# Kernel optimization log

Hardware: AMD Instinct MI355X
Metric: run time of the kernel (lower is better)

Reference implementation:

```python
import jax, jax.numpy as jnp
import numpy as np

T, B, E, H, DFF, K = 1024, 4, 512, 8, 2048, 31
D = E // H  # head_dim


def double_swish(x):
    # DoubleSwish: x * sigmoid(x - 1)
    return x * jax.nn.sigmoid(x - 1.0)


def ffn(x, w1, b1, w2, b2):
    # ScaledLinear -> ActivationBalancer(identity in eval) -> DoubleSwish -> ScaledLinear
    return double_swish(x @ w1.T + b1) @ w2.T + b2


def rel_shift(x):
    # x: (B, H, T, 2T-1) -> (B, H, T, T); out[b,h,i,j] = x[b,h,i, (T-1) - i + j]
    t = x.shape[2]
    idx = (t - 1) - jnp.arange(t)[:, None] + jnp.arange(t)[None, :]  # (T, T)
    return jnp.take_along_axis(x, idx[None, None], axis=-1)


def self_attn(x, pos_emb, wqkv, bqkv, wo, bo, wpos, u, v):
    # x: (T, B, E); Transformer-XL style rel-pos multi-head attention
    t, b, e = x.shape
    qkv = x @ wqkv.T + bqkv                       # (T, B, 3E)
    q, k, val = jnp.split(qkv, 3, axis=-1)
    q = q * (D ** -0.5)
    to_heads = lambda z: z.reshape(t, b, H, D).transpose(1, 2, 0, 3)  # (B,H,T,D)
    q, k, val = to_heads(q), to_heads(k), to_heads(val)
    # positional projection: (1, 2T-1, E) -> (1, H, D, 2T-1)
    p = (pos_emb @ wpos.T).reshape(1, 2 * t - 1, H, D).transpose(0, 2, 3, 1)
    ac = jnp.einsum('bhld,bhsd->bhls', q + u[None, :, None, :], k)
    bd = jnp.einsum('bhld,bhdm->bhlm', q + v[None, :, None, :], p)
    scores = ac + rel_shift(bd)                   # (B, H, T, T)
    attn = jax.nn.softmax(scores, axis=-1)
    out = jnp.einsum('bhls,bhsd->bhld', attn, val)
    out = out.transpose(2, 0, 1, 3).reshape(t, b, e)  # (T, B, E)
    return out @ wo.T + bo


def conv_module(x, pw1_w, pw1_b, dw_w, dw_b, pw2_w, pw2_b):
    # x: (T, B, C) -> (B, C, T)
    x = x.transpose(1, 2, 0)
    x = jnp.einsum('oc,bct->bot', pw1_w, x) + pw1_b[None, :, None]  # (B, 2C, T)
    a, g = jnp.split(x, 2, axis=1)
    x = a * jax.nn.sigmoid(g)                     # GLU over channel dim
    pad = (K - 1) // 2
    x = jax.lax.conv_general_dilated(
        x, dw_w, window_strides=(1,), padding=[(pad, pad)],
        dimension_numbers=('NCH', 'OIH', 'NCH'), feature_group_count=E)
    x = double_swish(x + dw_b[None, :, None])
    x = jnp.einsum('oc,bct->bot', pw2_w, x) + pw2_b[None, :, None]
    return x.transpose(2, 0, 1)                   # (T, B, C)


def basic_norm(x, log_eps):
    # BasicNorm: x * (mean(x^2, -1) + exp(eps))^{-0.5}
    return x * jax.lax.rsqrt(jnp.mean(x * x, axis=-1, keepdims=True) + jnp.exp(log_eps))


def setup_inputs() -> dict:
    key = jax.random.key(0)
    ks = jax.random.split(key, 24)
    std = jnp.float32(0.02)
    f = lambda k, s: jax.random.normal(k, s, jnp.float32)
    return dict(
        src=f(ks[0], (T, B, E)),
        pos_emb=f(ks[1], (1, 2 * T - 1, E)),
        in_proj_w=f(ks[2], (3 * E, E)) * std,
        in_proj_b=f(ks[3], (3 * E,)) * std,
        out_proj_w=f(ks[4], (E, E)) * std,
        out_proj_b=f(ks[5], (E,)) * std,
        linear_pos_w=f(ks[6], (E, E)) * std,
        pos_bias_u=f(ks[7], (H, D)) * jnp.float32(0.01),
        pos_bias_v=f(ks[8], (H, D)) * jnp.float32(0.01),
        ffm_w1=f(ks[9], (DFF, E)) * std, ffm_b1=f(ks[10], (DFF,)) * std,
        ffm_w2=f(ks[11], (E, DFF)) * std, ffm_b2=f(ks[12], (E,)) * std,
        ff_w1=f(ks[13], (DFF, E)) * std, ff_b1=f(ks[14], (DFF,)) * std,
        ff_w2=f(ks[15], (E, DFF)) * std, ff_b2=f(ks[16], (E,)) * std,
        conv_pw1_w=f(ks[17], (2 * E, E)) * std, conv_pw1_b=f(ks[18], (2 * E,)) * std,
        conv_dw_w=f(ks[19], (E, 1, K)) * std, conv_dw_b=f(ks[20], (E,)) * std,
        conv_pw2_w=f(ks[21], (E, E)) * std, conv_pw2_b=f(ks[22], (E,)) * std,
        norm_eps=jnp.array(np.log(0.25), jnp.float32),
    )


def reference(src, pos_emb, in_proj_w, in_proj_b, out_proj_w, out_proj_b,
              linear_pos_w, pos_bias_u, pos_bias_v,
              ffm_w1, ffm_b1, ffm_w2, ffm_b2,
              ff_w1, ff_b1, ff_w2, ff_b2,
              conv_pw1_w, conv_pw1_b, conv_dw_w, conv_dw_b, conv_pw2_w, conv_pw2_b,
              norm_eps):
    # macaron FFN
    x = src + ffn(src, ffm_w1, ffm_b1, ffm_w2, ffm_b2)
    # rel-pos self-attention
    x = x + self_attn(x, pos_emb, in_proj_w, in_proj_b, out_proj_w, out_proj_b,
                      linear_pos_w, pos_bias_u, pos_bias_v)
    # convolution module
    x = x + conv_module(x, conv_pw1_w, conv_pw1_b, conv_dw_w, conv_dw_b, conv_pw2_w, conv_pw2_b)
    # second FFN
    x = x + ffn(x, ff_w1, ff_b1, ff_w2, ff_b2)
    # balancer is identity in eval; final BasicNorm
    return basic_norm(x, norm_eps)
```

## Files before the change

kernel.cpp:

```cpp
#include <hip/hip_runtime.h>
#include <string.h>


#define T_ 1024
#define B_ 4
#define E_ 512
#define H_ 8
#define DFF_ 2048
#define KW_ 31

typedef unsigned short u16;
typedef unsigned int u32;
typedef __bf16 bf16x8 __attribute__((ext_vector_type(8)));
typedef float floatx4 __attribute__((ext_vector_type(4)));

__device__ __forceinline__ float b2f(u16 u) {
    return __uint_as_float(((u32)u) << 16);
}
__device__ __forceinline__ u16 f2b(float f) {
    u32 i = __float_as_uint(f);
    u32 r = (i + 0x7fffu + ((i >> 16) & 1u)) >> 16;
    return (u16)r;
}

__device__ __forceinline__ void glds16(const u16 *g, u16 *l) {
    __builtin_amdgcn_global_load_lds((const __attribute__((address_space(1))) void *)g,
                                     (__attribute__((address_space(3))) void *)l, 16, 0, 0);
}

__global__ __launch_bounds__(256) void fill_k(float *out, long long n, float val) {
    long long g = (long long)blockIdx.x * 256 + threadIdx.x;
    if (g < n) out[g] = val;
}

__global__ __launch_bounds__(256) void detect_k(const u16 *src16, int *flag) {
    __shared__ int sh[256];
    int tid = threadIdx.x;
    int cnt = 0;
    for (int i = tid; i < 4096; i += 256) {
        u16 x = src16[2 * i];
        int e = (x >> 7) & 0xFF;
        cnt += (e == 0 || (e >= 0x70 && e <= 0x8F)) ? 1 : 0;
    }
    sh[tid] = cnt;
    __syncthreads();
    for (int s = 128; s; s >>= 1) {
        if (tid < s) sh[tid] += sh[tid + s];
        __syncthreads();
    }
    if (tid == 0) *flag = (sh[0] < 2048) ? 1 : 0;
}

struct CVT {
    const void *in[24];
    long long pre[25];
};

__global__ __launch_bounds__(256) void convert_k(CVT c, u16 *dst, const int *flag,
                                                 long long total) {
    long long g = (long long)blockIdx.x * 256 + threadIdx.x;
    if (g >= total) return;
    int s = 0;
#pragma unroll
    for (int i = 1; i < 25; i++) s += (g >= c.pre[i]) ? 1 : 0;
    long long l = g - c.pre[s];
    int f = *flag;
    u16 v = f ? f2b(((const float *)c.in[s])[l]) : ((const u16 *)c.in[s])[l];
    dst[g] = v;
}

struct GP {
    const u16 *A, *B;
    u16 *C;
    const u16 *bias;
    const void *resin;
    float *xr;
    u16 *xb;
    const u16 *ub, *vb;
    u16 *qu, *qv, *kh, *vt;
    int M, N, K, lda, ldb, ldc, mode, qcols, resin_f32;
    float qscale;
};

__global__ __launch_bounds__(512) void gemm_nt(GP p) {
    __shared__ __align__(16) u16 As[3 * 4096];
    __shared__ __align__(16) u16 Bs[3 * 4096];
    const int tid = threadIdx.x;
    const int wv = tid >> 6, ln = tid & 63;
    const int l16 = ln & 15, quad = ln >> 4;
    const int wm = (wv >> 2) << 5;
    const int wn = (wv & 3) << 4;
    const int gx = gridDim.x;
    const int nb = gx * gridDim.y;
    const int lid = blockIdx.y * gx + blockIdx.x;
    const int nid = (lid & 7) * (nb >> 3) + (lid >> 3);
    const int m0 = (nid / gx) << 6, n0 = (nid % gx) << 6;
    floatx4 zero = {0.f, 0.f, 0.f, 0.f};
    floatx4 acc[2];
    acc[0] = zero;
    acc[1] = zero;

    const int NT = p.K >> 6;

    const int srow = tid >> 3;
    const int sg = ((tid & 7) ^ (srow & 7)) << 3;
    int ra = m0 + srow;
    if (ra > p.M - 1) ra = p.M - 1;
    const u16 *Agp = p.A + (long long)ra * p.lda + sg;
    const u16 *Bgp = p.B + (long long)(n0 + srow) * p.ldb + sg;

    auto stage = [&](int bidx, int t) {
        const int k0 = t << 6;
        const int o = bidx << 12;
        glds16(Agp + k0, As + o + tid * 8);
        glds16(Bgp + k0, Bs + o + tid * 8);
    };

    stage(0, 0);
    stage(1, 1);
    stage(2, 2);
    asm volatile("s_waitcnt vmcnt(4)" ::: "memory");
    __builtin_amdgcn_s_barrier();

    int cb = 0;
    for (int t = 0; t < NT; t++) {
        const int o = cb << 12;
#pragma unroll
        for (int kk = 0; kk < 2; kk++) {
            const int swz = ((((kk << 2) | quad) ^ (l16 & 7)) << 3);
            bf16x8 bfv = __builtin_bit_cast(bf16x8,
                *(const uint4 *)&Bs[o + ((wn + l16) << 6) + swz]);
#pragma unroll
            for (int mt = 0; mt < 2; mt++) {
                bf16x8 af = __builtin_bit_cast(bf16x8,
                    *(const uint4 *)&As[o + ((wm + (mt << 4) + l16) << 6) + swz]);
                acc[mt] = __builtin_amdgcn_mfma_f32_16x16x32_bf16(af, bfv, acc[mt], 0, 0, 0);
            }
        }
        if (t + 1 < NT) {
            __builtin_amdgcn_sched_barrier(0);
            __builtin_amdgcn_s_barrier();
            if (t + 3 < NT) {
                stage(cb, t + 3);
                asm volatile("s_waitcnt vmcnt(4)" ::: "memory");
            } else if (t + 2 < NT) {
                asm volatile("s_waitcnt vmcnt(2)" ::: "memory");
            } else {
                asm volatile("s_waitcnt vmcnt(0)" ::: "memory");
            }
            __builtin_amdgcn_s_barrier();
            __builtin_amdgcn_sched_barrier(0);
        }
        cb = (cb == 2) ? 0 : cb + 1;
    }

#pragma unroll
    for (int mt = 0; mt < 2; mt++) {
#pragma unroll
        for (int r = 0; r < 4; r++) {
            int gr = m0 + wm + (mt << 4) + (quad << 2) + r;
            int gc = n0 + wn + l16;
            bool oob = gr >= p.M;
            if (oob && p.mode != 3) continue;
            float y = 0.f;
            if (!oob) {
                y = acc[mt][r];
                if (p.bias) y += b2f(p.bias[gc]);
                if (gc < p.qcols) y *= p.qscale;
            }
            if (p.mode == 3) {
                p.C[((gc >> 6) << 17) + (gr << 6) + (gc & 63)] = f2b(y);
            } else if (p.mode == 0) {
                p.C[(long long)gr * p.ldc + gc] = f2b(y);
            } else if (p.mode == 1) {
                float s = 1.f / (1.f + __expf(1.f - y));
                p.C[(long long)gr * p.ldc + gc] = f2b(y * s);
            } else {
                long long idx = (long long)gr * p.ldc + gc;
                float rv = p.resin_f32 ? ((const float *)p.resin)[idx]
                                       : b2f(((const u16 *)p.resin)[idx]);
                float o = rv + y;
                p.xr[idx] = o;
                if (p.xb) p.xb[idx] = f2b(o);
            }
        }
    }
}

__global__ __launch_bounds__(512) void gemm_nt128(GP p) {
    __shared__ __align__(16) u16 As[3 * 4096];
    __shared__ __align__(16) u16 Bs[3 * 4096];
    const int tid = threadIdx.x;
    const int wv = tid >> 6, ln = tid & 63;
    const int l16 = ln & 15, quad = ln >> 4;
    const int wm = (wv >> 2) << 6;
    const int wn = (wv & 3) << 5;
    const int gx = gridDim.x;
    const int nb = gx * gridDim.y;
    const int lid = blockIdx.y * gx + blockIdx.x;
    const int nid = (lid & 7) * (nb >> 3) + (lid >> 3);
    const int m0 = (nid / gx) << 7, n0 = (nid % gx) << 7;
    const int srow = tid >> 2;
    const int sg = ((tid & 3) ^ ((tid >> 3) & 3)) << 3;
    const u16 *Agp = p.A + (long long)(m0 + srow) * p.lda + sg;
    const u16 *Bgp = p.B + (long long)(n0 + srow) * p.ldb + sg;
    floatx4 zero = {0.f, 0.f, 0.f, 0.f};
    floatx4 acc[4][2];
#pragma unroll
    for (int i = 0; i < 4; i++)
#pragma unroll
        for (int j = 0; j < 2; j++) acc[i][j] = zero;

    const int rswz = ((quad ^ ((l16 >> 1) & 3)) << 3);
    const int NT = p.K >> 5;

    auto stage = [&](int bidx, int t) {
        const int k0 = t << 5;
        const int o = bidx << 12;
        glds16(Agp + k0, As + o + tid * 8);
        glds16(Bgp + k0, Bs + o + tid * 8);
    };

    stage(0, 0);
    stage(1, 1);
    stage(2, 2);
    asm volatile("s_waitcnt vmcnt(4)" ::: "memory");
    __builtin_amdgcn_s_barrier();

    int cb = 0;
    for (int t = 0; t < NT; t++) {
        const int o = cb << 12;
        bf16x8 av[4], bv[2];
#pragma unroll
        for (int mt = 0; mt < 4; mt++)
            av[mt] = __builtin_bit_cast(bf16x8,
                *(const uint4 *)&As[o + ((wm + (mt << 4) + l16) << 5) + rswz]);
#pragma unroll
        for (int nt = 0; nt < 2; nt++)
            bv[nt] = __builtin_bit_cast(bf16x8,
                *(const uint4 *)&Bs[o + ((wn + (nt << 4) + l16) << 5) + rswz]);
#pragma unroll
        for (int mt = 0; mt < 4; mt++)
#pragma unroll
            for (int nt = 0; nt < 2; nt++)
                acc[mt][nt] = __builtin_amdgcn_mfma_f32_16x16x32_bf16(av[mt], bv[nt],
                                                                      acc[mt][nt], 0, 0, 0);
        if (t + 1 < NT) {
            __builtin_amdgcn_sched_barrier(0);
            __builtin_amdgcn_s_barrier();
            if (t + 3 < NT) {
                stage(cb, t + 3);
                asm volatile("s_waitcnt vmcnt(4)" ::: "memory");
            } else if (t + 2 < NT) {
                asm volatile("s_waitcnt vmcnt(2)" ::: "memory");
            } else {
                asm volatile("s_waitcnt vmcnt(0)" ::: "memory");
            }
            __builtin_amdgcn_s_barrier();
            __builtin_amdgcn_sched_barrier(0);
        }
        cb = (cb == 2) ? 0 : cb + 1;
    }

#pragma unroll
    for (int mt = 0; mt < 4; mt++)
#pragma unroll
        for (int nt = 0; nt < 2; nt++)
#pragma unroll
            for (int r = 0; r < 4; r++) {
                int gr = m0 + wm + (mt << 4) + (quad << 2) + r;
                int gc = n0 + wn + (nt << 4) + l16;
                float y = acc[mt][nt][r];
                if (p.bias) y += b2f(p.bias[gc]);
                if (gc < p.qcols) y *= p.qscale;
                if (p.mode == 0) {
                    p.C[(long long)gr * p.ldc + gc] = f2b(y);
                } else if (p.mode == 1) {
                    float s = 1.f / (1.f + __expf(1.f - y));
                    p.C[(long long)gr * p.ldc + gc] = f2b(y * s);
                } else if (p.mode == 4) {
                    int t = gr >> 2, b = gr & 3;
                    if (gc < E_) {
                        int z = b * 8 + (gc >> 6);
                        long long oq = ((long long)z << 16) + (t << 6) + (gc & 63);
                        p.qu[oq] = f2b(y + b2f(p.ub[gc]));
                        p.qv[oq] = f2b(y + b2f(p.vb[gc]));
                    } else if (gc < 2 * E_) {
                        int c = gc - E_;
                        int z = b * 8 + (c >> 6);
                        p.kh[((long long)z << 16) + (t << 6) + (c & 63)] = f2b(y);
                    } else {
                        int c = gc - 2 * E_;
                        int z = b * 8 + (c >> 6);
                        p.vt[(long long)((z << 6) + (c & 63)) * T_ + t] = f2b(y);
                    }
                } else {
                    long long idx = (long long)gr * p.ldc + gc;
                    float rv = p.resin_f32 ? ((const float *)p.resin)[idx]
                                           : b2f(((const u16 *)p.resin)[idx]);
                    float o = rv + y;
                    p.xr[idx] = o;
                    if (p.xb) p.xb[idx] = f2b(o);
                }
            }
}

__global__ __launch_bounds__(512) void gemm_glu(const u16 *A, const u16 *W, const u16 *bias,
                                                u16 *ch) {
    __shared__ __align__(16) u16 As[3 * 4096];
    __shared__ __align__(16) u16 Ba[3 * 4096];
    __shared__ __align__(16) u16 Bg[3 * 4096];
    const int tid = threadIdx.x;
    const int wv = tid >> 6, ln = tid & 63;
    const int l16 = ln & 15, quad = ln >> 4;
    const int wm = (wv >> 2) << 5;
    const int wn = (wv & 3) << 4;
    const int gx = gridDim.x;
    const int nb = gx * gridDim.y;
    const int lid = blockIdx.y * gx + blockIdx.x;
    const int nid = (lid & 7) * (nb >> 3) + (lid >> 3);
    const int m0 = (nid / gx) << 6, n0 = (nid % gx) << 6;
    floatx4 zero = {0.f, 0.f, 0.f, 0.f};
    floatx4 aa[2], ag[2];
    aa[0] = zero; aa[1] = zero; ag[0] = zero; ag[1] = zero;

    const int NT = 8;
    const int srow = tid >> 3;
    const int sg = ((tid & 7) ^ (srow & 7)) << 3;
    const u16 *Agp = A + ((long long)(m0 + srow) << 9) + sg;
    const u16 *Bap = W + ((long long)(n0 + srow) << 9) + sg;
    const u16 *Bgp = W + ((long long)(E_ + n0 + srow) << 9) + sg;

    auto stage = [&](int bidx, int t) {
        const int k0 = t << 6;
        const int o = bidx << 12;
        glds16(Agp + k0, As + o + tid * 8);
        glds16(Bap + k0, Ba + o + tid * 8);
        glds16(Bgp + k0, Bg + o + tid * 8);
    };

    stage(0, 0);
    stage(1, 1);
    stage(2, 2);
    asm volatile("s_waitcnt vmcnt(6)" ::: "memory");
    __builtin_amdgcn_s_barrier();

    int cb = 0;
    for (int t = 0; t < NT; t++) {
        const int o = cb << 12;
#pragma unroll
        for (int kk = 0; kk < 2; kk++) {
            const int swz = ((((kk << 2) | quad) ^ (l16 & 7)) << 3);
            bf16x8 ba = __builtin_bit_cast(bf16x8,
                *(const uint4 *)&Ba[o + ((wn + l16) << 6) + swz]);
            bf16x8 bg = __builtin_bit_cast(bf16x8,
                *(const uint4 *)&Bg[o + ((wn + l16) << 6) + swz]);
#pragma unroll
            for (int mt = 0; mt < 2; mt++) {
                bf16x8 af = __builtin_bit_cast(bf16x8,
                    *(const uint4 *)&As[o + ((wm + (mt << 4) + l16) << 6) + swz]);
                aa[mt] = __builtin_amdgcn_mfma_f32_16x16x32_bf16(af, ba, aa[mt], 0, 0, 0);
                ag[mt] = __builtin_amdgcn_mfma_f32_16x16x32_bf16(af, bg, ag[mt], 0, 0, 0);
            }
        }
        if (t + 1 < NT) {
            __builtin_amdgcn_sched_barrier(0);
            __builtin_amdgcn_s_barrier();
            if (t + 3 < NT) {
                stage(cb, t + 3);
                asm volatile("s_waitcnt vmcnt(6)" ::: "memory");
            } else if (t + 2 < NT) {
                asm volatile("s_waitcnt vmcnt(3)" ::: "memory");
            } else {
                asm volatile("s_waitcnt vmcnt(0)" ::: "memory");
            }
            __builtin_amdgcn_s_barrier();
            __builtin_amdgcn_sched_barrier(0);
        }
        cb = (cb == 2) ? 0 : cb + 1;
    }

#pragma unroll
    for (int mt = 0; mt < 2; mt++) {
#pragma unroll
        for (int r = 0; r < 4; r++) {
            int gr = m0 + wm + (mt << 4) + (quad << 2) + r;
            int gc = n0 + wn + l16;
            float a = aa[mt][r] + b2f(bias[gc]);
            float g = ag[mt][r] + b2f(bias[E_ + gc]);
            ch[((long long)gr << 9) + gc] = f2b(a * (1.f / (1.f + __expf(-g))));
        }
    }
}

struct FK {
    const u16 *QU, *QV, *KH, *PPH, *VT;
    u16 *attno;
};

__global__ __launch_bounds__(256) void flash_k(FK p) {
    __shared__ __align__(16) u16 lds[25088];
    u16 *Kh = lds;
    u16 *Ph = lds + 4096;
    u16 *Pb = lds + 20480;

    const int tid = threadIdx.x;
    const int wv = tid >> 6, ln = tid & 63;
    const int l16 = ln & 15, quad = ln >> 4;
    const int lid = blockIdx.y * 16 + blockIdx.x;
    const int nid = (lid & 7) * 64 + (lid >> 3);
    const int zg = nid >> 4;
    const int i0 = (nid & 15) << 6;
    const u16 *kh0 = p.KH + (long long)zg * 65536;
    const u16 *ph0 = p.PPH + (long long)(zg & 7) * 131072;
    const u16 *vt0 = p.VT + (long long)zg * 65536;

    auto stage_kp = [&](int jt) {
        const int j0 = jt << 6;
        const int m_start = 960 - i0 + j0;
#pragma unroll
        for (int ps = 0; ps < 2; ps++) {
            int g = ps * 256 + tid;
            int row = g >> 3;
            int src = ((g & 7) ^ (row & 7)) << 3;
            glds16(kh0 + ((j0 + row) << 6) + src, Kh + g * 8);
        }
#pragma unroll
        for (int ps = 0; ps < 4; ps++) {
            int g = ps * 256 + tid;
            int row = g >> 3;
            int src = ((g & 7) ^ (row & 7)) << 3;
            glds16(ph0 + ((m_start + row) << 6) + src, Ph + g * 8);
        }
    };
    auto stage_v = [&](int buf, int jt) {
        const int j0 = jt << 6;
        u16 *Vt = lds + 12288 + (buf << 12);
#pragma unroll
        for (int ps = 0; ps < 2; ps++) {
            int g = ps * 256 + tid;
            int row = g >> 3;
            int src = ((g & 7) ^ (row & 7)) << 3;
            glds16(vt0 + (row << 10) + j0 + src, Vt + g * 8);
        }
    };

    const long long qoff = (long long)zg * 65536 + (long long)(i0 + (wv << 4) + l16) * 64 + (quad << 3);
    bf16x8 aqu[2], aqv[2];
#pragma unroll
    for (int kk = 0; kk < 2; kk++) {
        aqu[kk] = __builtin_bit_cast(bf16x8, *(const uint4 *)(p.QU + qoff + (kk << 5)));
        aqv[kk] = __builtin_bit_cast(bf16x8, *(const uint4 *)(p.QV + qoff + (kk << 5)));
    }

    stage_kp(0);
    stage_v(0, 0);
    asm volatile("s_waitcnt vmcnt(0)" ::: "memory");
    __builtin_amdgcn_s_barrier();

    float lacc[4];
    floatx4 accO[4];
    floatx4 zero = {0.f, 0.f, 0.f, 0.f};
#pragma unroll
    for (int e = 0; e < 4; e++) lacc[e] = 0.f;
#pragma unroll
    for (int i = 0; i < 4; i++) accO[i] = zero;

    const int r16q = quad << 2;

    for (int jt = 0; jt < 16; jt++) {
        floatx4 aS[4], aB[5];
#pragma unroll
        for (int i = 0; i < 4; i++) aS[i] = zero;
#pragma unroll
        for (int i = 0; i < 5; i++) aB[i] = zero;
        __builtin_amdgcn_s_setprio(1);
#pragma unroll
        for (int kk = 0; kk < 2; kk++) {
            const int swz = ((((kk << 2) | quad) ^ (l16 & 7)) << 3);
#pragma unroll
            for (int nt = 0; nt < 4; nt++) {
                bf16x8 bf = __builtin_bit_cast(bf16x8,
                    *(const uint4 *)&Kh[(((nt << 4) | l16) << 6) + swz]);
                aS[nt] = __builtin_amdgcn_mfma_f32_16x16x32_bf16(aqu[kk], bf, aS[nt], 0, 0, 0);
            }
#pragma unroll
            for (int rt = 0; rt < 5; rt++) {
                bf16x8 bf = __builtin_bit_cast(bf16x8,
                    *(const uint4 *)&Ph[((((rt + 3 - wv) << 4) | l16) << 6) + swz]);
                aB[rt] = __builtin_amdgcn_mfma_f32_16x16x32_bf16(aqv[kk], bf, aB[rt], 0, 0, 0);
            }
        }
        __builtin_amdgcn_s_setprio(0);
        __builtin_amdgcn_sched_barrier(0);
        __builtin_amdgcn_s_barrier();
        if (jt + 1 < 16) {
            stage_kp(jt + 1);
            stage_v((jt + 1) & 1, jt + 1);
        }
        __builtin_amdgcn_sched_barrier(0);

#pragma unroll
        for (int e = 0; e < 4; e++) {
            const int r16 = r16q + e;
            const int t = l16 + 15 - r16;
            const int srcl = (quad << 4) | (t & 15);
            const int carry = t >> 4;
            float s5[5];
#pragma unroll
            for (int rt = 0; rt < 5; rt++) s5[rt] = __shfl(aB[rt][e], srcl, 64);
            float ps = 0.f;
#pragma unroll
            for (int nt = 0; nt < 4; nt++) {
                float bd = carry ? s5[nt + 1] : s5[nt];
                float pe = __expf(aS[nt][e] + bd);
                ps += pe;
                Pb[(((wv << 4) + r16) * 72) + (nt << 4) + l16] = f2b(pe);
            }
            lacc[e] += ps;
        }

        const u16 *Vt = lds + 12288 + ((jt & 1) << 12);
        __builtin_amdgcn_s_setprio(1);
#pragma unroll
        for (int kk = 0; kk < 2; kk++) {
            const int swz = ((((kk << 2) | quad) ^ (l16 & 7)) << 3);
            bf16x8 ap = __builtin_bit_cast(bf16x8,
                *(const uint4 *)&Pb[(((wv << 4) | l16) * 72) + (kk << 5) + (quad << 3)]);
#pragma unroll
            for (int nd = 0; nd < 4; nd++) {
                bf16x8 bv = __builtin_bit_cast(bf16x8,
                    *(const uint4 *)&Vt[(((nd << 4) | l16) << 6) + swz]);
                accO[nd] = __builtin_amdgcn_mfma_f32_16x16x32_bf16(ap, bv, accO[nd], 0, 0, 0);
            }
        }
        __builtin_amdgcn_s_setprio(0);

        if (jt + 1 < 16) {
            __builtin_amdgcn_sched_barrier(0);
            asm volatile("s_waitcnt vmcnt(0)" ::: "memory");
            __builtin_amdgcn_s_barrier();
            __builtin_amdgcn_sched_barrier(0);
        }
    }

    const int b = zg >> 3, h = zg & 7;
#pragma unroll
    for (int e = 0; e < 4; e++) {
#pragma unroll
        for (int msk = 1; msk < 16; msk <<= 1) lacc[e] += __shfl_xor(lacc[e], msk, 64);
        float inv = 1.f / lacc[e];
        int t = i0 + (wv << 4) + (quad << 2) + e;
#pragma unroll
        for (int nd = 0; nd < 4; nd++) {
            int d = (nd << 4) + l16;
            p.attno[(long long)(t * B_ + b) * E_ + h * 64 + d] = f2b(accO[nd][e] * inv);
        }
    }
}


__global__ __launch_bounds__(256) void dwconv_k(const u16 *ch, const u16 *w, const u16 *bias,
                                                u16 *cd) {
    const int cp = threadIdx.x;
    const int b = blockIdx.x >> 7;
    const int t0 = (blockIdx.x & 127) << 3;
    const int c0 = cp << 1;
    float in0[38], in1[38];
#pragma unroll
    for (int j = 0; j < 38; j++) {
        int tt = t0 - 15 + j;
        u32 v = 0;
        if (tt >= 0 && tt < T_) v = *(const u32 *)&ch[tt * 2048 + b * 512 + c0];
        in0[j] = b2f((u16)(v & 0xffff));
        in1[j] = b2f((u16)(v >> 16));
    }
    float w0[KW_], w1[KW_];
#pragma unroll
    for (int kk = 0; kk < KW_; kk++) {
        w0[kk] = b2f(w[c0 * KW_ + kk]);
        w1[kk] = b2f(w[c0 * KW_ + KW_ + kk]);
    }
    float bi0 = b2f(bias[c0]), bi1 = b2f(bias[c0 + 1]);
#pragma unroll
    for (int t = 0; t < 8; t++) {
        float a0 = bi0, a1 = bi1;
#pragma unroll
        for (int kk = 0; kk < KW_; kk++) {
            a0 += in0[t + kk] * w0[kk];
            a1 += in1[t + kk] * w1[kk];
        }
        float s0 = 1.f / (1.f + __expf(1.f - a0));
        float s1 = 1.f / (1.f + __expf(1.f - a1));
        u32 o = (u32)f2b(a0 * s0) | ((u32)f2b(a1 * s1) << 16);
        *(u32 *)&cd[(t0 + t) * 2048 + b * 512 + c0] = o;
    }
}

__global__ __launch_bounds__(256) void norm_k(const float *xr, const float *epsp, float *out) {
    int wv = threadIdx.x >> 6, ln = threadIdx.x & 63;
    long long row = blockIdx.x * 4 + wv;
    const float *x = xr + row * E_;
    float vals[8], ss = 0.f;
#pragma unroll
    for (int i = 0; i < 8; i++) {
        vals[i] = x[ln + (i << 6)];
        ss += vals[i] * vals[i];
    }
#pragma unroll
    for (int m = 32; m; m >>= 1) ss += __shfl_xor(ss, m, 64);
    float sc = rsqrtf(ss * (1.f / (float)E_) + __expf(epsp[0]));
    float *o = out + row * E_;
#pragma unroll
    for (int i = 0; i < 8; i++) o[ln + (i << 6)] = vals[i] * sc;
}


extern "C" void kernel_launch(void *const *d_in, const int *in_sizes, int n_in,
                              void *d_out, int out_size, void *d_ws, size_t ws_size,
                              hipStream_t stream) {
    const size_t MB = (size_t)1 << 20;
    static const long long EXPECT[24] = {
        2097152, 1048064, 786432, 1536, 262144, 512, 262144, 512, 512,
        1048576, 2048, 1048576, 512, 1048576, 2048, 1048576, 512,
        524288, 1024, 15872, 512, 262144, 512, 1};
    const size_t NEED = 93 * MB;

    float code = 0.f;
    if (n_in != 24) {
        code = 1000.f + (float)n_in;
    } else {
        for (int i = 0; i < 24; i++) {
            if ((long long)in_sizes[i] != EXPECT[i]) { code = 2000.f + 64.f * i; break; }
        }
    }
    if (code == 0.f && out_size != 2097152) code = 3000.f;
    if (code == 0.f && ws_size < NEED) code = 5000.f + (float)(ws_size / MB);
    if (code != 0.f) {
        long long n = (long long)out_size;
        fill_k<<<dim3((unsigned)((n + 255) / 256)), dim3(256), 0, stream>>>((float *)d_out, n, code);
        return;
    }

    char *w = (char *)d_ws;
    int *flag = (int *)(w + 0);
    u16 *cv = (u16 *)(w + 1 * MB);
    float *xr = (float *)(w + 21 * MB);
    u16 *xb = (u16 *)(w + 29 * MB);
    u16 *h1 = (u16 *)(w + 33 * MB);
    u16 *pph = (u16 *)(w + 63 * MB);
    u16 *QU = (u16 *)(w + 65 * MB);
    u16 *QV = (u16 *)(w + 69 * MB);
    u16 *KH = (u16 *)(w + 73 * MB);
    u16 *VT = (u16 *)(w + 77 * MB);
    u16 *attno = (u16 *)(w + 81 * MB);
    u16 *ch = (u16 *)(w + 85 * MB);
    u16 *cd = (u16 *)(w + 89 * MB);

    detect_k<<<dim3(1), dim3(256), 0, stream>>>((const u16 *)d_in[0], flag);
    CVT c;
    c.pre[0] = 0;
    for (int i = 0; i < 24; i++) {
        c.in[i] = d_in[i];
        c.pre[i + 1] = c.pre[i] + in_sizes[i];
    }
    long long total = c.pre[24];
    convert_k<<<dim3((unsigned)((total + 255) / 256)), dim3(256), 0, stream>>>(c, cv, flag, total);

    const u16 *src = cv + c.pre[0];
    const u16 *pos_emb = cv + c.pre[1];
    const u16 *w_qkv = cv + c.pre[2];
    const u16 *b_qkv = cv + c.pre[3];
    const u16 *w_o = cv + c.pre[4];
    const u16 *b_o = cv + c.pre[5];
    const u16 *w_pos = cv + c.pre[6];
    const u16 *u_bias = cv + c.pre[7];
    const u16 *v_bias = cv + c.pre[8];
    const u16 *ffm_w1 = cv + c.pre[9];
    const u16 *ffm_b1 = cv + c.pre[10];
    const u16 *ffm_w2 = cv + c.pre[11];
    const u16 *ffm_b2 = cv + c.pre[12];
    const u16 *ff_w1 = cv + c.pre[13];
    const u16 *ff_b1 = cv + c.pre[14];
    const u16 *ff_w2 = cv + c.pre[15];
    const u16 *ff_b2 = cv + c.pre[16];
    const u16 *pw1_w = cv + c.pre[17];
    const u16 *pw1_b = cv + c.pre[18];
    const u16 *dw_w = cv + c.pre[19];
    const u16 *dw_b = cv + c.pre[20];
    const u16 *pw2_w = cv + c.pre[21];
    const u16 *pw2_b = cv + c.pre[22];

    auto mk = [](const void *A, int lda, const void *B, int ldb, void *C, int ldc,
                 const void *bias, int M, int N, int K, int mode) {
        GP p;
        memset(&p, 0, sizeof(p));
        p.A = (const u16 *)A; p.B = (const u16 *)B; p.C = (u16 *)C; p.bias = (const u16 *)bias;
        p.M = M; p.N = N; p.K = K; p.lda = lda; p.ldb = ldb; p.ldc = ldc; p.mode = mode;
        p.qscale = 1.f;
        return p;
    };
    auto launch = [&](GP p) {
        dim3 g((p.N + 63) / 64, (p.M + 63) / 64, 1);
        gemm_nt<<<g, dim3(512), 0, stream>>>(p);
    };
    auto launch128 = [&](GP p) {
        dim3 g(p.N >> 7, p.M >> 7, 1);
        gemm_nt128<<<g, dim3(512), 0, stream>>>(p);
    };

    const int M = T_ * B_;

    { GP p = mk(src, E_, ffm_w1, E_, h1, DFF_, ffm_b1, M, DFF_, E_, 1); launch128(p); }
    { GP p = mk(h1, DFF_, ffm_w2, DFF_, nullptr, E_, ffm_b2, M, E_, DFF_, 2);
      p.resin = d_in[0]; p.resin_f32 = 1; p.xr = xr; p.xb = xb; launch(p); }

    { GP p = mk(xb, E_, w_qkv, E_, nullptr, 3 * E_, b_qkv, M, 3 * E_, E_, 4);
      p.qcols = E_; p.qscale = 0.125f;
      p.ub = u_bias; p.vb = v_bias; p.qu = QU; p.qv = QV; p.kh = KH; p.vt = VT;
      launch128(p); }
    { GP p = mk(pos_emb, E_, w_pos, E_, pph, E_, nullptr, 2 * T_ - 1, E_, E_, 3); launch(p); }

    {
        FK f;
        f.QU = QU; f.QV = QV; f.KH = KH; f.PPH = pph; f.VT = VT; f.attno = attno;
        flash_k<<<dim3(16, 32), dim3(256), 0, stream>>>(f);
    }

    { GP p = mk(attno, E_, w_o, E_, nullptr, E_, b_o, M, E_, E_, 2);
      p.resin = xr; p.resin_f32 = 1; p.xr = xr; p.xb = xb; launch(p); }

    gemm_glu<<<dim3(8, 64), dim3(512), 0, stream>>>(xb, pw1_w, pw1_b, ch);
    dwconv_k<<<dim3(512), dim3(256), 0, stream>>>(ch, dw_w, dw_b, cd);
    { GP p = mk(cd, E_, pw2_w, E_, nullptr, E_, pw2_b, M, E_, E_, 2);
      p.resin = xr; p.resin_f32 = 1; p.xr = xr; p.xb = xb; launch(p); }

    { GP p = mk(xb, E_, ff_w1, E_, h1, DFF_, ff_b1, M, DFF_, E_, 1); launch128(p); }
    { GP p = mk(h1, DFF_, ff_w2, DFF_, nullptr, E_, ff_b2, M, E_, DFF_, 2);
      p.resin = xr; p.resin_f32 = 1; p.xr = xr; p.xb = nullptr; launch(p); }

    norm_k<<<dim3(M / 4), dim3(256), 0, stream>>>(xr, (const float *)d_in[23], (float *)d_out);
}
```

Before: 373.1 us.

## Split attention KV range across two blocks and combine partials

The flash attention kernel now splits the 1024 keys into two halves handled by separate blocks, doubling the grid to 1024 blocks. Each block writes unnormalised fp32 partial outputs and row sums, and a new combine kernel adds the halves and normalises. The positional tile is now loaded straight from global memory into registers instead of through LDS, and K/V staging is issued at the top of each iteration. This raises occupancy and parallelism on a grid that was small relative to the CU count, at the cost of an extra launch and a round trip of partial results through memory. Reusing the h1 buffer for the partials relies on h1 being dead at that point.

Result: slower. 411.8 us (+10.4%).

```diff
diff --git a/kernel.cpp b/kernel.cpp
--- a/kernel.cpp
+++ b/kernel.cpp
@@ -395,54 +395,58 @@
 
 struct FK {
     const u16 *QU, *QV, *KH, *PPH, *VT;
-    u16 *attno;
+    float *Op;
+    float *lp;
 };
 
 __global__ __launch_bounds__(256) void flash_k(FK p) {
-    __shared__ __align__(16) u16 lds[25088];
-    u16 *Kh = lds;
-    u16 *Ph = lds + 4096;
-    u16 *Pb = lds + 20480;
+    __shared__ __align__(16) u16 lds[20992];
+    u16 *Pb = lds + 16384;
 
     const int tid = threadIdx.x;
     const int wv = tid >> 6, ln = tid & 63;
     const int l16 = ln & 15, quad = ln >> 4;
-    const int lid = blockIdx.y * 16 + blockIdx.x;
-    const int nid = (lid & 7) * 64 + (lid >> 3);
-    const int zg = nid >> 4;
+    const int lid = blockIdx.y * 32 + blockIdx.x;
+    const int nid = (lid & 7) * 128 + (lid >> 3);
+    const int zg = nid >> 5;
+    const int kvh = (nid >> 4) & 1;
     const int i0 = (nid & 15) << 6;
+    const int jt0 = kvh << 3;
     const u16 *kh0 = p.KH + (long long)zg * 65536;
     const u16 *ph0 = p.PPH + (long long)(zg & 7) * 131072;
     const u16 *vt0 = p.VT + (long long)zg * 65536;
 
-    auto stage_kp = [&](int jt) {
+    auto stage_k = [&](int buf, int jt) {
         const int j0 = jt << 6;
-        const int m_start = 960 - i0 + j0;
 #pragma unroll
         for (int ps = 0; ps < 2; ps++) {
             int g = ps * 256 + tid;
             int row = g >> 3;
             int src = ((g & 7) ^ (row & 7)) << 3;
-            glds16(kh0 + ((j0 + row) << 6) + src, Kh + g * 8);
-        }
-#pragma unroll
-        for (int ps = 0; ps < 4; ps++) {
-            int g = ps * 256 + tid;
-            int row = g >> 3;
-            int src = ((g & 7) ^ (row & 7)) << 3;
-            glds16(ph0 + ((m_start + row) << 6) + src, Ph + g * 8);
+            glds16(kh0 + ((j0 + row) << 6) + src, lds + (buf << 12) + g * 8);
         }
     };
     auto stage_v = [&](int buf, int jt) {
         const int j0 = jt << 6;
-        u16 *Vt = lds + 12288 + (buf << 12);
 #pragma unroll
         for (int ps = 0; ps < 2; ps++) {
             int g = ps * 256 + tid;
             int row = g >> 3;
             int src = ((g & 7) ^ (row & 7)) << 3;
-            glds16(vt0 + (row << 10) + j0 + src, Vt + g * 8);
-        }
+            glds16(vt0 + (row << 10) + j0 + src, lds + 8192 + (buf << 12) + g * 8);
+        }
+    };
+
+    uint4 pf[10];
+    auto load_ph = [&](int jt) {
+        const int m_start = 960 - i0 + (jt << 6);
+        const u16 *base = ph0 + ((long long)(m_start + l16) << 6) + (quad << 3);
+#pragma unroll
+        for (int rt = 0; rt < 5; rt++)
+#pragma unroll
+            for (int kk = 0; kk < 2; kk++)
+                pf[rt * 2 + kk] = *(const uint4 *)(base +
+                    (((rt + 3 - wv) << 4) << 6) + (kk << 5));
     };
 
     const long long qoff = (long long)zg * 65536 + (long long)(i0 + (wv << 4) + l16) * 64 + (quad << 3);
@@ -453,8 +457,9 @@
         aqv[kk] = __builtin_bit_cast(bf16x8, *(const uint4 *)(p.QV + qoff + (kk << 5)));
     }
 
-    stage_kp(0);
-    stage_v(0, 0);
+    stage_k(0, jt0);
+    stage_v(0, jt0);
+    load_ph(jt0);
     asm volatile("s_waitcnt vmcnt(0)" ::: "memory");
     __builtin_amdgcn_s_barrier();
 
@@ -468,7 +473,16 @@
 
     const int r16q = quad << 2;
 
-    for (int jt = 0; jt < 16; jt++) {
+    for (int jt = jt0; jt < jt0 + 8; jt++) {
+        const int buf = jt & 1;
+        if (jt + 1 < jt0 + 8) {
+            stage_k(buf ^ 1, jt + 1);
+            stage_v(buf ^ 1, jt + 1);
+        }
+        __builtin_amdgcn_sched_barrier(0);
+        const u16 *Kh = lds + (buf << 12);
+        const u16 *Vt = lds + 8192 + (buf << 12);
+
         floatx4 aS[4], aB[5];
 #pragma unroll
         for (int i = 0; i < 4; i++) aS[i] = zero;
@@ -486,18 +500,13 @@
             }
 #pragma unroll
             for (int rt = 0; rt < 5; rt++) {
-                bf16x8 bf = __builtin_bit_cast(bf16x8,
-                    *(const uint4 *)&Ph[((((rt + 3 - wv) << 4) | l16) << 6) + swz]);
+                bf16x8 bf = __builtin_bit_cast(bf16x8, pf[rt * 2 + kk]);
                 aB[rt] = __builtin_amdgcn_mfma_f32_16x16x32_bf16(aqv[kk], bf, aB[rt], 0, 0, 0);
             }
         }
         __builtin_amdgcn_s_setprio(0);
         __builtin_amdgcn_sched_barrier(0);
-        __builtin_amdgcn_s_barrier();
-        if (jt + 1 < 16) {
-            stage_kp(jt + 1);
-            stage_v((jt + 1) & 1, jt + 1);
-        }
+        if (jt + 1 < jt0 + 8) load_ph(jt + 1);
         __builtin_amdgcn_sched_barrier(0);
 
 #pragma unroll
@@ -520,7 +529,6 @@
             lacc[e] += ps;
         }
 
-        const u16 *Vt = lds + 12288 + ((jt & 1) << 12);
         __builtin_amdgcn_s_setprio(1);
 #pragma unroll
         for (int kk = 0; kk < 2; kk++) {
@@ -536,7 +544,7 @@
         }
         __builtin_amdgcn_s_setprio(0);
 
-        if (jt + 1 < 16) {
+        if (jt + 1 < jt0 + 8) {
             __builtin_amdgcn_sched_barrier(0);
             asm volatile("s_waitcnt vmcnt(0)" ::: "memory");
             __builtin_amdgcn_s_barrier();
@@ -544,19 +552,25 @@
         }
     }
 
-    const int b = zg >> 3, h = zg & 7;
 #pragma unroll
     for (int e = 0; e < 4; e++) {
 #pragma unroll
         for (int msk = 1; msk < 16; msk <<= 1) lacc[e] += __shfl_xor(lacc[e], msk, 64);
-        float inv = 1.f / lacc[e];
         int t = i0 + (wv << 4) + (quad << 2) + e;
-#pragma unroll
-        for (int nd = 0; nd < 4; nd++) {
-            int d = (nd << 4) + l16;
-            p.attno[(long long)(t * B_ + b) * E_ + h * 64 + d] = f2b(accO[nd][e] * inv);
-        }
-    }
+        float *op = p.Op + ((((long long)kvh << 5) + zg) * 1024 + t) * 64;
+#pragma unroll
+        for (int nd = 0; nd < 4; nd++) op[(nd << 4) + l16] = accO[nd][e];
+        if (l16 == 0) p.lp[(((kvh << 5) + zg) << 10) + t] = lacc[e];
+    }
+}
+
+__global__ __launch_bounds__(256) void combine_k(const float *Op, const float *lp,
+                                                 u16 *attno) {
+    int gid = blockIdx.x * 256 + threadIdx.x;
+    int z = gid >> 16, rem = gid & 65535, t = rem >> 6, d = rem & 63;
+    float o = Op[gid] + Op[gid + (1 << 21)];
+    float l = lp[(z << 10) + t] + lp[(1 << 15) + (z << 10) + t];
+    attno[(long long)((t << 2) + (z >> 3)) * E_ + ((z & 7) << 6) + d] = f2b(o / l);
 }
 
 
@@ -648,6 +662,8 @@
     float *xr = (float *)(w + 21 * MB);
     u16 *xb = (u16 *)(w + 29 * MB);
     u16 *h1 = (u16 *)(w + 33 * MB);
+    float *Opart = (float *)(w + 33 * MB);
+    float *lpart = (float *)(w + 49 * MB);
     u16 *pph = (u16 *)(w + 63 * MB);
     u16 *QU = (u16 *)(w + 65 * MB);
     u16 *QV = (u16 *)(w + 69 * MB);
@@ -723,8 +739,10 @@
 
     {
         FK f;
-        f.QU = QU; f.QV = QV; f.KH = KH; f.PPH = pph; f.VT = VT; f.attno = attno;
-        flash_k<<<dim3(16, 32), dim3(256), 0, stream>>>(f);
+        f.QU = QU; f.QV = QV; f.KH = KH; f.PPH = pph; f.VT = VT;
+        f.Op = Opart; f.lp = lpart;
+        flash_k<<<dim3(32, 32), dim3(256), 0, stream>>>(f);
+        combine_k<<<dim3(8192), dim3(256), 0, stream>>>(Opart, lpart, attno);
     }
 
     { GP p = mk(attno, E_, w_o, E_, nullptr, E_, b_o, M, E_, E_, 2);
```

## Double-buffer K, V and P tiles in flash attention kernel

Applied to the files above, without the earlier changes.

Gives the K, positional-projection and V tiles full double buffering in LDS, so the next tile's global-to-LDS loads are issued at the top of each iteration, before the QK/QP MFMAs, instead of after them. This removes the mid-iteration barrier and lets the loads overlap the whole iteration's compute. In exchange, LDS use rises from about 49 KB to about 74 KB per block, which may lower occupancy, and an extra barrier is added at the end of each iteration.

New measurement: 390.6 us. 1.05x slower.

```diff
diff --git a/kernel.cpp b/kernel.cpp
--- a/kernel.cpp
+++ b/kernel.cpp
@@ -399,10 +399,7 @@
 };
 
 __global__ __launch_bounds__(256) void flash_k(FK p) {
-    __shared__ __align__(16) u16 lds[25088];
-    u16 *Kh = lds;
-    u16 *Ph = lds + 4096;
-    u16 *Pb = lds + 20480;
+    __shared__ __align__(16) u16 lds[2 * 16384 + 4608];
 
     const int tid = threadIdx.x;
     const int wv = tid >> 6, ln = tid & 63;
@@ -414,16 +411,21 @@
     const u16 *kh0 = p.KH + (long long)zg * 65536;
     const u16 *ph0 = p.PPH + (long long)(zg & 7) * 131072;
     const u16 *vt0 = p.VT + (long long)zg * 65536;
-
-    auto stage_kp = [&](int jt) {
+    u16 *Pb = lds + 32768;
+
+    auto stage = [&](int buf, int jt) {
         const int j0 = jt << 6;
         const int m_start = 960 - i0 + j0;
+        u16 *Kh = lds + (buf << 14);
+        u16 *Vt = Kh + 4096;
+        u16 *Ph = Kh + 8192;
 #pragma unroll
         for (int ps = 0; ps < 2; ps++) {
             int g = ps * 256 + tid;
             int row = g >> 3;
             int src = ((g & 7) ^ (row & 7)) << 3;
             glds16(kh0 + ((j0 + row) << 6) + src, Kh + g * 8);
+            glds16(vt0 + (row << 10) + j0 + src, Vt + g * 8);
         }
 #pragma unroll
         for (int ps = 0; ps < 4; ps++) {
@@ -433,17 +435,6 @@
             glds16(ph0 + ((m_start + row) << 6) + src, Ph + g * 8);
         }
     };
-    auto stage_v = [&](int buf, int jt) {
-        const int j0 = jt << 6;
-        u16 *Vt = lds + 12288 + (buf << 12);
-#pragma unroll
-        for (int ps = 0; ps < 2; ps++) {
-            int g = ps * 256 + tid;
-            int row = g >> 3;
-            int src = ((g & 7) ^ (row & 7)) << 3;
-            glds16(vt0 + (row << 10) + j0 + src, Vt + g * 8);
-        }
-    };
 
     const long long qoff = (long long)zg * 65536 + (long long)(i0 + (wv << 4) + l16) * 64 + (quad << 3);
     bf16x8 aqu[2], aqv[2];
@@ -453,8 +444,7 @@
         aqv[kk] = __builtin_bit_cast(bf16x8, *(const uint4 *)(p.QV + qoff + (kk << 5)));
     }
 
-    stage_kp(0);
-    stage_v(0, 0);
+    stage(0, 0);
     asm volatile("s_waitcnt vmcnt(0)" ::: "memory");
     __builtin_amdgcn_s_barrier();
 
@@ -469,6 +459,13 @@
     const int r16q = quad << 2;
 
     for (int jt = 0; jt < 16; jt++) {
+        if (jt + 1 < 16) stage((jt + 1) & 1, jt + 1);
+        __builtin_amdgcn_sched_barrier(0);
+        const int o = (jt & 1) << 14;
+        const u16 *Kh = lds + o;
+        const u16 *Vt = lds + o + 4096;
+        const u16 *Ph = lds + o + 8192;
+
         floatx4 aS[4], aB[5];
 #pragma unroll
         for (int i = 0; i < 4; i++) aS[i] = zero;
@@ -492,13 +489,6 @@
             }
         }
         __builtin_amdgcn_s_setprio(0);
-        __builtin_amdgcn_sched_barrier(0);
-        __builtin_amdgcn_s_barrier();
-        if (jt + 1 < 16) {
-            stage_kp(jt + 1);
-            stage_v((jt + 1) & 1, jt + 1);
-        }
-        __builtin_amdgcn_sched_barrier(0);
 
 #pragma unroll
         for (int e = 0; e < 4; e++) {
@@ -520,7 +510,6 @@
             lacc[e] += ps;
         }
 
-        const u16 *Vt = lds + 12288 + ((jt & 1) << 12);
         __builtin_amdgcn_s_setprio(1);
 #pragma unroll
         for (int kk = 0; kk < 2; kk++) {
@@ -538,6 +527,7 @@
 
         if (jt + 1 < 16) {
             __builtin_amdgcn_sched_barrier(0);
+            __builtin_amdgcn_s_barrier();
             asm volatile("s_waitcnt vmcnt(0)" ::: "memory");
             __builtin_amdgcn_s_barrier();
             __builtin_amdgcn_sched_barrier(0);
```
